# Performance work log

Hardware: AMD Instinct MI355X
Metric: run time of the kernel (lower is better)

## Reference

```python
import jax, jax.numpy as jnp
import numpy as np

N_NODES = 10000
N_EDGES = 640000
IN_FEATS = 128
H_FEATS1 = 128
NUM_OUTPUTS = 64


def setup_inputs() -> dict:
    key = jax.random.key(0)
    k0, k1, k2, k3, k4 = jax.random.split(key, 5)
    in_feat = jax.random.normal(k0, (N_NODES, IN_FEATS), dtype=jnp.float32)
    src = jax.random.randint(k1, (N_EDGES,), 0, N_NODES, dtype=jnp.int64)
    dst = jax.random.randint(k2, (N_EDGES,), 0, N_NODES, dtype=jnp.int64)
    W1 = jax.random.normal(k3, (IN_FEATS, H_FEATS1), dtype=jnp.float32) * 0.05
    b1 = jnp.zeros((H_FEATS1,), dtype=jnp.float32)
    W2 = jax.random.normal(k4, (H_FEATS1, NUM_OUTPUTS), dtype=jnp.float32) * 0.05
    b2 = jnp.zeros((NUM_OUTPUTS,), dtype=jnp.float32)
    return {"in_feat": in_feat, "src": src, "dst": dst,
            "W1": W1, "b1": b1, "W2": W2, "b2": b2}


def _graph_conv(src, dst, x, W, b):
    # DGL GraphConv with norm='both': out = D_out^{-1/2} A^T-agg D_in^{-1/2} x W + b
    n = x.shape[0]
    ones = jnp.ones((src.shape[0],), dtype=x.dtype)
    deg_out = jnp.clip(jax.ops.segment_sum(ones, src, num_segments=n), 1.0)
    deg_in = jnp.clip(jax.ops.segment_sum(ones, dst, num_segments=n), 1.0)
    h = x * jax.lax.rsqrt(deg_out)[:, None]            # src-side normalization
    agg = jax.ops.segment_sum(h[src], dst, num_segments=n)  # SpMM: sum over in-edges
    agg = agg * jax.lax.rsqrt(deg_in)[:, None]         # dst-side normalization
    return agg @ W + b


def reference(in_feat, src, dst, W1, b1, W2, b2):
    h = _graph_conv(src, dst, in_feat, W1, b1)
    h = jax.nn.relu(h)  # dropout=0 -> identity
    return _graph_conv(src, dst, h, W2, b2)
```

## Files before the change

kernel.cpp:

```cpp
#include <hip/hip_runtime.h>

#define NFEAT 128
#define NOUT  64
#define PCAP  128
#define HB    256

__global__ void hist_kernel(const int* __restrict__ src, const int* __restrict__ dst,
                            unsigned short* __restrict__ hist_src,
                            unsigned short* __restrict__ hist_dst,
                            unsigned int* __restrict__ pe, int nN, int nE) {
    extern __shared__ int bins[];
    int b = blockIdx.x;
    int per = (nE + HB - 1) / HB;
    int lo = b * per, hi = min(lo + per, nE);
    for (int i = threadIdx.x; i < nN; i += blockDim.x) bins[i] = 0;
    __syncthreads();
    for (int e = lo + threadIdx.x; e < hi; e += blockDim.x) {
        int s = src[e], d = dst[e];
        atomicAdd(&bins[d], 1);
        atomicAdd(&bins[s], 0x10000);
        pe[e] = (unsigned int)(unsigned short)s | ((unsigned int)d << 16);
    }
    __syncthreads();
    for (int i = threadIdx.x; i < nN; i += blockDim.x) {
        int v = bins[i];
        hist_dst[(size_t)b * nN + i] = (unsigned short)(v & 0xFFFF);
        hist_src[(size_t)b * nN + i] = (unsigned short)(v >> 16);
    }
}

__global__ void offsets_kernel(const unsigned short* __restrict__ hist_src,
                               const unsigned short* __restrict__ hist_dst,
                               unsigned short* __restrict__ base_rel,
                               unsigned short* __restrict__ deg_in,
                               float* __restrict__ rs_in, float* __restrict__ rs_out, int nN) {
    int tid = blockIdx.x * blockDim.x + threadIdx.x;
    if (tid < nN) {
        int i = tid;
        int run = 0;
#pragma unroll 16
        for (int b = 0; b < HB; b++) {
            base_rel[(size_t)b * nN + i] = (unsigned short)run;
            run += hist_dst[(size_t)b * nN + i];
        }
        deg_in[i] = (unsigned short)min(run, PCAP);
        rs_in[i] = rsqrtf(fmaxf((float)run, 1.0f));
    } else if (tid < 2 * nN) {
        int i = tid - nN;
        int to = 0;
#pragma unroll 16
        for (int b = 0; b < HB; b++) to += hist_src[(size_t)b * nN + i];
        rs_out[i] = rsqrtf(fmaxf((float)to, 1.0f));
    }
}

__global__ void scatter_kernel(const unsigned int* __restrict__ pe,
                               const unsigned short* __restrict__ base_rel,
                               unsigned short* __restrict__ csr, int nN, int nE) {
    extern __shared__ int cur[];
    int b = blockIdx.x;
    int per = (nE + HB - 1) / HB;
    int lo = b * per, hi = min(lo + per, nE);
    for (int i = threadIdx.x; i < nN; i += blockDim.x)
        cur[i] = base_rel[(size_t)b * nN + i];
    __syncthreads();
    for (int e = lo + threadIdx.x; e < hi; e += blockDim.x) {
        unsigned int v = pe[e];
        int s = v & 0xFFFF, d = v >> 16;
        int pos = atomicAdd(&cur[d], 1);
        if (pos < PCAP)
            csr[(size_t)d * PCAP + pos] = (unsigned short)s;
    }
}

__global__ void gather1_kernel(const unsigned short* __restrict__ deg_in,
                               const unsigned short* __restrict__ csr,
                               const float* __restrict__ x, const float* __restrict__ rs_out,
                               const float* __restrict__ rs_in,
                               float* __restrict__ t, int nN) {
    __shared__ unsigned short eids[4][PCAP];
    __shared__ float rsv[4][PCAP];
    int tid = threadIdx.x;
    int w = tid >> 6, lane = tid & 63;
    int i = blockIdx.x * 4 + w;
    int n = deg_in[i];
    ((unsigned int*)eids[w])[lane] = ((const unsigned int*)(csr + (size_t)i * PCAP))[lane];
    for (int e = lane; e < n; e += 64) rsv[w][e] = rs_out[eids[w][e]];

    const float4* xv = (const float4*)x;
    int quad = lane >> 4;
    int g = lane & 15;
    float s_in = rs_in[i];
#pragma unroll
    for (int p = 0; p < 2; p++) {
        int gg = g + 16 * p;
        float4 acc = {0.f, 0.f, 0.f, 0.f};
        int e = quad;
        for (; e + 28 < n; e += 32) {
            float4 vv[8]; float ff[8];
#pragma unroll
            for (int u = 0; u < 8; u++) {
                int s = eids[w][e + 4 * u];
                ff[u] = rsv[w][e + 4 * u];
                vv[u] = xv[(size_t)s * 32 + gg];
            }
#pragma unroll
            for (int u = 0; u < 8; u++) {
                acc.x += vv[u].x * ff[u];
                acc.y += vv[u].y * ff[u];
                acc.z += vv[u].z * ff[u];
                acc.w += vv[u].w * ff[u];
            }
        }
        for (; e + 12 < n; e += 16) {
            float4 vv[4]; float ff[4];
#pragma unroll
            for (int u = 0; u < 4; u++) {
                int s = eids[w][e + 4 * u];
                ff[u] = rsv[w][e + 4 * u];
                vv[u] = xv[(size_t)s * 32 + gg];
            }
#pragma unroll
            for (int u = 0; u < 4; u++) {
                acc.x += vv[u].x * ff[u];
                acc.y += vv[u].y * ff[u];
                acc.z += vv[u].z * ff[u];
                acc.w += vv[u].w * ff[u];
            }
        }
        for (; e < n; e += 4) {
            int s0 = eids[w][e];
            float f0 = rsv[w][e];
            float4 v0 = xv[(size_t)s0 * 32 + gg];
            acc.x += v0.x * f0; acc.y += v0.y * f0; acc.z += v0.z * f0; acc.w += v0.w * f0;
        }
#pragma unroll
        for (int d = 16; d <= 32; d <<= 1) {
            acc.x += __shfl_xor(acc.x, d);
            acc.y += __shfl_xor(acc.y, d);
            acc.z += __shfl_xor(acc.z, d);
            acc.w += __shfl_xor(acc.w, d);
        }
        if (lane < 16) {
            acc.x *= s_in; acc.y *= s_in; acc.z *= s_in; acc.w *= s_in;
            ((float4*)(t + (size_t)i * NFEAT))[gg] = acc;
        }
    }
}

#define NPB 16
__global__ void mlp_kernel(const float* __restrict__ t_in, const float* __restrict__ rs_out,
                           const float* __restrict__ W1, const float* __restrict__ b1,
                           const float* __restrict__ W2, float* __restrict__ z, int nN) {
    __shared__ float ts[NPB][NFEAT];
    __shared__ float h1[NPB][NFEAT];
    int i0 = blockIdx.x * NPB;
    int tid = threadIdx.x;
    for (int t2 = tid; t2 < NPB * NFEAT; t2 += 256)
        ts[t2 >> 7][t2 & 127] = t_in[(size_t)i0 * NFEAT + t2];
    __syncthreads();
    {
        int j = tid & 127;
        int g = (tid >> 7) * 8;
        float a[8];
        float b = b1[j];
#pragma unroll
        for (int u = 0; u < 8; u++) a[u] = b;
#pragma unroll 8
        for (int k = 0; k < NFEAT; k++) {
            float w = W1[k * NFEAT + j];
#pragma unroll
            for (int u = 0; u < 8; u++) a[u] += ts[g + u][k] * w;
        }
#pragma unroll
        for (int u = 0; u < 8; u++) h1[g + u][j] = fmaxf(a[u], 0.0f);
    }
    __syncthreads();
    {
        int j2 = tid & 63;
        int g2 = (tid >> 6) * 4;
        float c[4] = {0.f, 0.f, 0.f, 0.f};
#pragma unroll 8
        for (int k = 0; k < NFEAT; k++) {
            float w = W2[k * NOUT + j2];
#pragma unroll
            for (int u = 0; u < 4; u++) c[u] += h1[g2 + u][k] * w;
        }
#pragma unroll
        for (int u = 0; u < 4; u++)
            z[(size_t)(i0 + g2 + u) * NOUT + j2] = c[u] * rs_out[i0 + g2 + u];
    }
}

__global__ void gather2_kernel(const unsigned short* __restrict__ deg_in,
                               const unsigned short* __restrict__ csr,
                               const float* __restrict__ z, const float* __restrict__ rs_in,
                               const float* __restrict__ b2, float* __restrict__ out, int nN) {
    __shared__ unsigned short eids[4][PCAP];
    int tid = threadIdx.x;
    int w = tid >> 6, lane = tid & 63;
    int i = blockIdx.x * 4 + w;
    int n = deg_in[i];
    ((unsigned int*)eids[w])[lane] = ((const unsigned int*)(csr + (size_t)i * PCAP))[lane];

    const float4* zv = (const float4*)z;
    int quad = lane >> 4;
    int g = lane & 15;
    float4 acc = {0.f, 0.f, 0.f, 0.f};
    int e = quad;
    for (; e + 28 < n; e += 32) {
        float4 vv[8];
#pragma unroll
        for (int u = 0; u < 8; u++) {
            int s = eids[w][e + 4 * u];
            vv[u] = zv[(size_t)s * 16 + g];
        }
#pragma unroll
        for (int u = 0; u < 8; u++) {
            acc.x += vv[u].x; acc.y += vv[u].y; acc.z += vv[u].z; acc.w += vv[u].w;
        }
    }
    for (; e + 12 < n; e += 16) {
        float4 vv[4];
#pragma unroll
        for (int u = 0; u < 4; u++) {
            int s = eids[w][e + 4 * u];
            vv[u] = zv[(size_t)s * 16 + g];
        }
#pragma unroll
        for (int u = 0; u < 4; u++) {
            acc.x += vv[u].x; acc.y += vv[u].y; acc.z += vv[u].z; acc.w += vv[u].w;
        }
    }
    for (; e < n; e += 4) {
        float4 v0 = zv[(size_t)eids[w][e] * 16 + g];
        acc.x += v0.x; acc.y += v0.y; acc.z += v0.z; acc.w += v0.w;
    }
#pragma unroll
    for (int d = 16; d <= 32; d <<= 1) {
        acc.x += __shfl_xor(acc.x, d);
        acc.y += __shfl_xor(acc.y, d);
        acc.z += __shfl_xor(acc.z, d);
        acc.w += __shfl_xor(acc.w, d);
    }
    if (lane < 16) {
        float s = rs_in[i];
        float4 bb = ((const float4*)b2)[g];
        acc.x = acc.x * s + bb.x; acc.y = acc.y * s + bb.y;
        acc.z = acc.z * s + bb.z; acc.w = acc.w * s + bb.w;
        ((float4*)(out + (size_t)i * NOUT))[g] = acc;
    }
}

extern "C" void kernel_launch(void* const* d_in, const int* in_sizes, int n_in,
                              void* d_out, int out_size, void* d_ws, size_t ws_size,
                              hipStream_t stream) {
    const float* x  = (const float*)d_in[0];
    const int* src  = (const int*)d_in[1];
    const int* dst  = (const int*)d_in[2];
    const float* W1 = (const float*)d_in[3];
    const float* b1 = (const float*)d_in[4];
    const float* W2 = (const float*)d_in[5];
    const float* b2 = (const float*)d_in[6];
    float* out = (float*)d_out;

    const int nN = in_sizes[0] / NFEAT;
    const int nE = in_sizes[1];

    char* p = (char*)d_ws;
    unsigned short* hist_src = (unsigned short*)p; p += (size_t)HB * nN * 2;
    unsigned short* hist_dst = (unsigned short*)p; p += (size_t)HB * nN * 2;
    unsigned short* base_rel = (unsigned short*)p; p += (size_t)HB * nN * 2;
    unsigned int*   pe       = (unsigned int*)p;   p += (size_t)nE * 4;
    unsigned short* csr      = (unsigned short*)p; p += (size_t)nN * PCAP * 2;
    unsigned short* deg_in   = (unsigned short*)p; p += (size_t)nN * 2;
    float* rs_in  = (float*)p; p += (size_t)nN * sizeof(float);
    float* rs_out = (float*)p; p += (size_t)nN * sizeof(float);
    float* t = (float*)p; p += (size_t)nN * NFEAT * sizeof(float);
    float* z = (float*)p; p += (size_t)nN * NOUT * sizeof(float);

    hist_kernel<<<HB, 256, (size_t)nN * sizeof(int), stream>>>(
        src, dst, hist_src, hist_dst, pe, nN, nE);
    offsets_kernel<<<(2 * nN + 255) / 256, 256, 0, stream>>>(
        hist_src, hist_dst, base_rel, deg_in, rs_in, rs_out, nN);
    scatter_kernel<<<HB, 256, (size_t)nN * sizeof(int), stream>>>(
        pe, base_rel, csr, nN, nE);
    gather1_kernel<<<nN / 4, 256, 0, stream>>>(deg_in, csr, x, rs_out, rs_in, t, nN);
    mlp_kernel<<<nN / NPB, 256, 0, stream>>>(t, rs_out, W1, b1, W2, z, nN);
    gather2_kernel<<<nN / 4, 256, 0, stream>>>(deg_in, csr, z, rs_in, b2, out, nN);
}
```

Measured before the change: 160.3 us.

## Build CSR with global atomics in one pass, replacing histogram/offsets/scatter pipeline

Replaces the three-kernel, block-local histogram, prefix and scatter CSR construction with a memset plus a single kernel. That kernel does global atomic increments on the in and out degree arrays and writes each source index into a fixed-capacity per-destination slot. The rsqrt degree normalizations are now computed on the fly in the gather and MLP kernels instead of being precomputed. This removes two launches and large per-block histogram traffic, at the cost of contended global atomics. Neighbor order within each row also becomes nondeterministic, which changes the float summation order.

```diff
diff --git a/kernel.cpp b/kernel.cpp
--- a/kernel.cpp
+++ b/kernel.cpp
@@ -3,94 +3,39 @@
 #define NFEAT 128
 #define NOUT  64
 #define PCAP  128
-#define HB    256
-
-__global__ void hist_kernel(const int* __restrict__ src, const int* __restrict__ dst,
-                            unsigned short* __restrict__ hist_src,
-                            unsigned short* __restrict__ hist_dst,
-                            unsigned int* __restrict__ pe, int nN, int nE) {
-    extern __shared__ int bins[];
-    int b = blockIdx.x;
-    int per = (nE + HB - 1) / HB;
-    int lo = b * per, hi = min(lo + per, nE);
-    for (int i = threadIdx.x; i < nN; i += blockDim.x) bins[i] = 0;
-    __syncthreads();
-    for (int e = lo + threadIdx.x; e < hi; e += blockDim.x) {
+
+__global__ void build_kernel(const int* __restrict__ src, const int* __restrict__ dst,
+                             int* __restrict__ deg_in, int* __restrict__ deg_out,
+                             unsigned short* __restrict__ csr, int nE) {
+    int e = blockIdx.x * blockDim.x + threadIdx.x;
+    if (e < nE) {
         int s = src[e], d = dst[e];
-        atomicAdd(&bins[d], 1);
-        atomicAdd(&bins[s], 0x10000);
-        pe[e] = (unsigned int)(unsigned short)s | ((unsigned int)d << 16);
-    }
-    __syncthreads();
-    for (int i = threadIdx.x; i < nN; i += blockDim.x) {
-        int v = bins[i];
-        hist_dst[(size_t)b * nN + i] = (unsigned short)(v & 0xFFFF);
-        hist_src[(size_t)b * nN + i] = (unsigned short)(v >> 16);
-    }
-}
-
-__global__ void offsets_kernel(const unsigned short* __restrict__ hist_src,
-                               const unsigned short* __restrict__ hist_dst,
-                               unsigned short* __restrict__ base_rel,
-                               unsigned short* __restrict__ deg_in,
-                               float* __restrict__ rs_in, float* __restrict__ rs_out, int nN) {
-    int tid = blockIdx.x * blockDim.x + threadIdx.x;
-    if (tid < nN) {
-        int i = tid;
-        int run = 0;
-#pragma unroll 16
-        for (int b = 0; b < HB; b++) {
-            base_rel[(size_t)b * nN + i] = (unsigned short)run;
-            run += hist_dst[(size_t)b * nN + i];
-        }
-        deg_in[i] = (unsigned short)min(run, PCAP);
-        rs_in[i] = rsqrtf(fmaxf((float)run, 1.0f));
-    } else if (tid < 2 * nN) {
-        int i = tid - nN;
-        int to = 0;
-#pragma unroll 16
-        for (int b = 0; b < HB; b++) to += hist_src[(size_t)b * nN + i];
-        rs_out[i] = rsqrtf(fmaxf((float)to, 1.0f));
-    }
-}
-
-__global__ void scatter_kernel(const unsigned int* __restrict__ pe,
-                               const unsigned short* __restrict__ base_rel,
-                               unsigned short* __restrict__ csr, int nN, int nE) {
-    extern __shared__ int cur[];
-    int b = blockIdx.x;
-    int per = (nE + HB - 1) / HB;
-    int lo = b * per, hi = min(lo + per, nE);
-    for (int i = threadIdx.x; i < nN; i += blockDim.x)
-        cur[i] = base_rel[(size_t)b * nN + i];
-    __syncthreads();
-    for (int e = lo + threadIdx.x; e < hi; e += blockDim.x) {
-        unsigned int v = pe[e];
-        int s = v & 0xFFFF, d = v >> 16;
-        int pos = atomicAdd(&cur[d], 1);
+        atomicAdd(&deg_out[s], 1);
+        int pos = atomicAdd(&deg_in[d], 1);
         if (pos < PCAP)
             csr[(size_t)d * PCAP + pos] = (unsigned short)s;
     }
 }
 
-__global__ void gather1_kernel(const unsigned short* __restrict__ deg_in,
+__global__ void gather1_kernel(const int* __restrict__ deg_in, const int* __restrict__ deg_out,
                                const unsigned short* __restrict__ csr,
-                               const float* __restrict__ x, const float* __restrict__ rs_out,
-                               const float* __restrict__ rs_in,
+                               const float* __restrict__ x,
                                float* __restrict__ t, int nN) {
     __shared__ unsigned short eids[4][PCAP];
     __shared__ float rsv[4][PCAP];
     int tid = threadIdx.x;
     int w = tid >> 6, lane = tid & 63;
     int i = blockIdx.x * 4 + w;
-    int n = deg_in[i];
+    int nf = deg_in[i];
+    int n = min(nf, PCAP);
+    float s_in = rsqrtf(fmaxf((float)nf, 1.0f));
     ((unsigned int*)eids[w])[lane] = ((const unsigned int*)(csr + (size_t)i * PCAP))[lane];
-    for (int e = lane; e < n; e += 64) rsv[w][e] = rs_out[eids[w][e]];
+    for (int e = lane; e < n; e += 64)
+        rsv[w][e] = rsqrtf(fmaxf((float)deg_out[eids[w][e]], 1.0f));
 
     const float4* xv = (const float4*)x;
     int quad = lane >> 4;
     int g = lane & 15;
-    float s_in = rs_in[i];
 #pragma unroll
     for (int p = 0; p < 2; p++) {
         int gg = g + 16 * p;
@@ -149,7 +94,7 @@
 }
 
 #define NPB 16
-__global__ void mlp_kernel(const float* __restrict__ t_in, const float* __restrict__ rs_out,
+__global__ void mlp_kernel(const float* __restrict__ t_in, const int* __restrict__ deg_out,
                            const float* __restrict__ W1, const float* __restrict__ b1,
                            const float* __restrict__ W2, float* __restrict__ z, int nN) {
     __shared__ float ts[NPB][NFEAT];
@@ -187,20 +132,23 @@
             for (int u = 0; u < 4; u++) c[u] += h1[g2 + u][k] * w;
         }
 #pragma unroll
-        for (int u = 0; u < 4; u++)
-            z[(size_t)(i0 + g2 + u) * NOUT + j2] = c[u] * rs_out[i0 + g2 + u];
-    }
-}
-
-__global__ void gather2_kernel(const unsigned short* __restrict__ deg_in,
+        for (int u = 0; u < 4; u++) {
+            float rs = rsqrtf(fmaxf((float)deg_out[i0 + g2 + u], 1.0f));
+            z[(size_t)(i0 + g2 + u) * NOUT + j2] = c[u] * rs;
+        }
+    }
+}
+
+__global__ void gather2_kernel(const int* __restrict__ deg_in,
                                const unsigned short* __restrict__ csr,
-                               const float* __restrict__ z, const float* __restrict__ rs_in,
+                               const float* __restrict__ z,
                                const float* __restrict__ b2, float* __restrict__ out, int nN) {
     __shared__ unsigned short eids[4][PCAP];
     int tid = threadIdx.x;
     int w = tid >> 6, lane = tid & 63;
     int i = blockIdx.x * 4 + w;
-    int n = deg_in[i];
+    int nf = deg_in[i];
+    int n = min(nf, PCAP);
     ((unsigned int*)eids[w])[lane] = ((const unsigned int*)(csr + (size_t)i * PCAP))[lane];
 
     const float4* zv = (const float4*)z;
@@ -244,7 +192,7 @@
         acc.w += __shfl_xor(acc.w, d);
     }
     if (lane < 16) {
-        float s = rs_in[i];
+        float s = rsqrtf(fmaxf((float)nf, 1.0f));
         float4 bb = ((const float4*)b2)[g];
         acc.x = acc.x * s + bb.x; acc.y = acc.y * s + bb.y;
         acc.z = acc.z * s + bb.z; acc.w = acc.w * s + bb.w;
@@ -268,24 +216,15 @@
     const int nE = in_sizes[1];
 
     char* p = (char*)d_ws;
-    unsigned short* hist_src = (unsigned short*)p; p += (size_t)HB * nN * 2;
-    unsigned short* hist_dst = (unsigned short*)p; p += (size_t)HB * nN * 2;
-    unsigned short* base_rel = (unsigned short*)p; p += (size_t)HB * nN * 2;
-    unsigned int*   pe       = (unsigned int*)p;   p += (size_t)nE * 4;
-    unsigned short* csr      = (unsigned short*)p; p += (size_t)nN * PCAP * 2;
-    unsigned short* deg_in   = (unsigned short*)p; p += (size_t)nN * 2;
-    float* rs_in  = (float*)p; p += (size_t)nN * sizeof(float);
-    float* rs_out = (float*)p; p += (size_t)nN * sizeof(float);
+    int* deg_in  = (int*)p; p += (size_t)nN * sizeof(int);
+    int* deg_out = (int*)p; p += (size_t)nN * sizeof(int);
+    unsigned short* csr = (unsigned short*)p; p += (size_t)nN * PCAP * 2;
     float* t = (float*)p; p += (size_t)nN * NFEAT * sizeof(float);
     float* z = (float*)p; p += (size_t)nN * NOUT * sizeof(float);
 
-    hist_kernel<<<HB, 256, (size_t)nN * sizeof(int), stream>>>(
-        src, dst, hist_src, hist_dst, pe, nN, nE);
-    offsets_kernel<<<(2 * nN + 255) / 256, 256, 0, stream>>>(
-        hist_src, hist_dst, base_rel, deg_in, rs_in, rs_out, nN);
-    scatter_kernel<<<HB, 256, (size_t)nN * sizeof(int), stream>>>(
-        pe, base_rel, csr, nN, nE);
-    gather1_kernel<<<nN / 4, 256, 0, stream>>>(deg_in, csr, x, rs_out, rs_in, t, nN);
-    mlp_kernel<<<nN / NPB, 256, 0, stream>>>(t, rs_out, W1, b1, W2, z, nN);
-    gather2_kernel<<<nN / 4, 256, 0, stream>>>(deg_in, csr, z, rs_in, b2, out, nN);
-}
+    hipMemsetAsync(d_ws, 0, 2 * (size_t)nN * sizeof(int), stream);
+    build_kernel<<<(nE + 255) / 256, 256, 0, stream>>>(src, dst, deg_in, deg_out, csr, nE);
+    gather1_kernel<<<nN / 4, 256, 0, stream>>>(deg_in, deg_out, csr, x, t, nN);
+    mlp_kernel<<<nN / NPB, 256, 0, stream>>>(t, deg_out, W1, b1, W2, z, nN);
+    gather2_kernel<<<nN / 4, 256, 0, stream>>>(deg_in, csr, z, b2, out, nN);
+}
```

Measured after the change: 179.4 us. +11.9%, slower.

## Store gathered node features in fp16 to halve gather traffic

Applied to the files above, without the earlier changes.

Converts the input features to fp16 inside the histogram kernel and has the MLP write its per-node output in fp16. Both gather kernels then read half as many bytes per edge, with each lane handling eight values instead of four and accumulating in fp32. This targets memory bandwidth in the two SpMM gathers, which are random-access and bandwidth-bound. The trade is reduced precision in the aggregated features and an extra conversion pass over x in the first kernel.

```diff
diff --git a/kernel.cpp b/kernel.cpp
--- a/kernel.cpp
+++ b/kernel.cpp
@@ -1,4 +1,5 @@
 #include <hip/hip_runtime.h>
+#include <hip/hip_fp16.h>
 
 #define NFEAT 128
 #define NOUT  64
@@ -8,7 +9,9 @@
 __global__ void hist_kernel(const int* __restrict__ src, const int* __restrict__ dst,
                             unsigned short* __restrict__ hist_src,
                             unsigned short* __restrict__ hist_dst,
-                            unsigned int* __restrict__ pe, int nN, int nE) {
+                            unsigned int* __restrict__ pe,
+                            const float* __restrict__ x, uint4* __restrict__ xh,
+                            int nN, int nE) {
     extern __shared__ int bins[];
     int b = blockIdx.x;
     int per = (nE + HB - 1) / HB;
@@ -26,6 +29,14 @@
         int v = bins[i];
         hist_dst[(size_t)b * nN + i] = (unsigned short)(v & 0xFFFF);
         hist_src[(size_t)b * nN + i] = (unsigned short)(v >> 16);
+    }
+    const float4* xf = (const float4*)x;
+    int nchunk = nN * NFEAT / 8;
+    for (int c = blockIdx.x * blockDim.x + threadIdx.x; c < nchunk; c += gridDim.x * blockDim.x) {
+        float4 a = xf[2 * c], bb = xf[2 * c + 1];
+        __half2 h[4] = {__floats2half2_rn(a.x, a.y),  __floats2half2_rn(a.z, a.w),
+                        __floats2half2_rn(bb.x, bb.y), __floats2half2_rn(bb.z, bb.w)};
+        xh[c] = *(uint4*)h;
     }
 }
 
@@ -73,9 +84,17 @@
     }
 }
 
+__device__ __forceinline__ void fma8(float* acc, uint4 v, float f) {
+    const __half2* h = (const __half2*)&v;
+    float2 p0 = __half22float2(h[0]), p1 = __half22float2(h[1]);
+    float2 p2 = __half22float2(h[2]), p3 = __half22float2(h[3]);
+    acc[0] += p0.x * f; acc[1] += p0.y * f; acc[2] += p1.x * f; acc[3] += p1.y * f;
+    acc[4] += p2.x * f; acc[5] += p2.y * f; acc[6] += p3.x * f; acc[7] += p3.y * f;
+}
+
 __global__ void gather1_kernel(const unsigned short* __restrict__ deg_in,
                                const unsigned short* __restrict__ csr,
-                               const float* __restrict__ x, const float* __restrict__ rs_out,
+                               const uint4* __restrict__ xh, const float* __restrict__ rs_out,
                                const float* __restrict__ rs_in,
                                float* __restrict__ t, int nN) {
     __shared__ unsigned short eids[4][PCAP];
@@ -87,71 +106,52 @@
     ((unsigned int*)eids[w])[lane] = ((const unsigned int*)(csr + (size_t)i * PCAP))[lane];
     for (int e = lane; e < n; e += 64) rsv[w][e] = rs_out[eids[w][e]];
 
-    const float4* xv = (const float4*)x;
     int quad = lane >> 4;
     int g = lane & 15;
     float s_in = rs_in[i];
-#pragma unroll
-    for (int p = 0; p < 2; p++) {
-        int gg = g + 16 * p;
-        float4 acc = {0.f, 0.f, 0.f, 0.f};
-        int e = quad;
-        for (; e + 28 < n; e += 32) {
-            float4 vv[8]; float ff[8];
-#pragma unroll
-            for (int u = 0; u < 8; u++) {
-                int s = eids[w][e + 4 * u];
-                ff[u] = rsv[w][e + 4 * u];
-                vv[u] = xv[(size_t)s * 32 + gg];
-            }
-#pragma unroll
-            for (int u = 0; u < 8; u++) {
-                acc.x += vv[u].x * ff[u];
-                acc.y += vv[u].y * ff[u];
-                acc.z += vv[u].z * ff[u];
-                acc.w += vv[u].w * ff[u];
-            }
-        }
-        for (; e + 12 < n; e += 16) {
-            float4 vv[4]; float ff[4];
-#pragma unroll
-            for (int u = 0; u < 4; u++) {
-                int s = eids[w][e + 4 * u];
-                ff[u] = rsv[w][e + 4 * u];
-                vv[u] = xv[(size_t)s * 32 + gg];
-            }
-#pragma unroll
-            for (int u = 0; u < 4; u++) {
-                acc.x += vv[u].x * ff[u];
-                acc.y += vv[u].y * ff[u];
-                acc.z += vv[u].z * ff[u];
-                acc.w += vv[u].w * ff[u];
-            }
-        }
-        for (; e < n; e += 4) {
-            int s0 = eids[w][e];
-            float f0 = rsv[w][e];
-            float4 v0 = xv[(size_t)s0 * 32 + gg];
-            acc.x += v0.x * f0; acc.y += v0.y * f0; acc.z += v0.z * f0; acc.w += v0.w * f0;
-        }
-#pragma unroll
-        for (int d = 16; d <= 32; d <<= 1) {
-            acc.x += __shfl_xor(acc.x, d);
-            acc.y += __shfl_xor(acc.y, d);
-            acc.z += __shfl_xor(acc.z, d);
-            acc.w += __shfl_xor(acc.w, d);
-        }
-        if (lane < 16) {
-            acc.x *= s_in; acc.y *= s_in; acc.z *= s_in; acc.w *= s_in;
-            ((float4*)(t + (size_t)i * NFEAT))[gg] = acc;
-        }
+    float acc[8] = {0.f, 0.f, 0.f, 0.f, 0.f, 0.f, 0.f, 0.f};
+    int e = quad;
+    for (; e + 28 < n; e += 32) {
+        uint4 vv[8]; float ff[8];
+#pragma unroll
+        for (int u = 0; u < 8; u++) {
+            int s = eids[w][e + 4 * u];
+            ff[u] = rsv[w][e + 4 * u];
+            vv[u] = xh[(size_t)s * 16 + g];
+        }
+#pragma unroll
+        for (int u = 0; u < 8; u++) fma8(acc, vv[u], ff[u]);
+    }
+    for (; e + 12 < n; e += 16) {
+        uint4 vv[4]; float ff[4];
+#pragma unroll
+        for (int u = 0; u < 4; u++) {
+            int s = eids[w][e + 4 * u];
+            ff[u] = rsv[w][e + 4 * u];
+            vv[u] = xh[(size_t)s * 16 + g];
+        }
+#pragma unroll
+        for (int u = 0; u < 4; u++) fma8(acc, vv[u], ff[u]);
+    }
+    for (; e < n; e += 4) {
+        fma8(acc, xh[(size_t)eids[w][e] * 16 + g], rsv[w][e]);
+    }
+#pragma unroll
+    for (int d = 16; d <= 32; d <<= 1)
+#pragma unroll
+        for (int k = 0; k < 8; k++) acc[k] += __shfl_xor(acc[k], d);
+    if (lane < 16) {
+        float4 o0 = {acc[0] * s_in, acc[1] * s_in, acc[2] * s_in, acc[3] * s_in};
+        float4 o1 = {acc[4] * s_in, acc[5] * s_in, acc[6] * s_in, acc[7] * s_in};
+        float4* tp = (float4*)(t + (size_t)i * NFEAT + g * 8);
+        tp[0] = o0; tp[1] = o1;
     }
 }
 
 #define NPB 16
 __global__ void mlp_kernel(const float* __restrict__ t_in, const float* __restrict__ rs_out,
                            const float* __restrict__ W1, const float* __restrict__ b1,
-                           const float* __restrict__ W2, float* __restrict__ z, int nN) {
+                           const float* __restrict__ W2, __half* __restrict__ zh, int nN) {
     __shared__ float ts[NPB][NFEAT];
     __shared__ float h1[NPB][NFEAT];
     int i0 = blockIdx.x * NPB;
@@ -188,13 +188,13 @@
         }
 #pragma unroll
         for (int u = 0; u < 4; u++)
-            z[(size_t)(i0 + g2 + u) * NOUT + j2] = c[u] * rs_out[i0 + g2 + u];
+            zh[(size_t)(i0 + g2 + u) * NOUT + j2] = __float2half_rn(c[u] * rs_out[i0 + g2 + u]);
     }
 }
 
 __global__ void gather2_kernel(const unsigned short* __restrict__ deg_in,
                                const unsigned short* __restrict__ csr,
-                               const float* __restrict__ z, const float* __restrict__ rs_in,
+                               const uint4* __restrict__ zh, const float* __restrict__ rs_in,
                                const float* __restrict__ b2, float* __restrict__ out, int nN) {
     __shared__ unsigned short eids[4][PCAP];
     int tid = threadIdx.x;
@@ -203,52 +203,38 @@
     int n = deg_in[i];
     ((unsigned int*)eids[w])[lane] = ((const unsigned int*)(csr + (size_t)i * PCAP))[lane];
 
-    const float4* zv = (const float4*)z;
-    int quad = lane >> 4;
-    int g = lane & 15;
-    float4 acc = {0.f, 0.f, 0.f, 0.f};
-    int e = quad;
-    for (; e + 28 < n; e += 32) {
-        float4 vv[8];
-#pragma unroll
-        for (int u = 0; u < 8; u++) {
-            int s = eids[w][e + 4 * u];
-            vv[u] = zv[(size_t)s * 16 + g];
-        }
-#pragma unroll
-        for (int u = 0; u < 8; u++) {
-            acc.x += vv[u].x; acc.y += vv[u].y; acc.z += vv[u].z; acc.w += vv[u].w;
-        }
-    }
-    for (; e + 12 < n; e += 16) {
-        float4 vv[4];
-#pragma unroll
-        for (int u = 0; u < 4; u++) {
-            int s = eids[w][e + 4 * u];
-            vv[u] = zv[(size_t)s * 16 + g];
-        }
-#pragma unroll
-        for (int u = 0; u < 4; u++) {
-            acc.x += vv[u].x; acc.y += vv[u].y; acc.z += vv[u].z; acc.w += vv[u].w;
-        }
-    }
-    for (; e < n; e += 4) {
-        float4 v0 = zv[(size_t)eids[w][e] * 16 + g];
-        acc.x += v0.x; acc.y += v0.y; acc.z += v0.z; acc.w += v0.w;
-    }
-#pragma unroll
-    for (int d = 16; d <= 32; d <<= 1) {
-        acc.x += __shfl_xor(acc.x, d);
-        acc.y += __shfl_xor(acc.y, d);
-        acc.z += __shfl_xor(acc.z, d);
-        acc.w += __shfl_xor(acc.w, d);
-    }
-    if (lane < 16) {
+    int oct = lane >> 3;
+    int g = lane & 7;
+    float acc[8] = {0.f, 0.f, 0.f, 0.f, 0.f, 0.f, 0.f, 0.f};
+    int e = oct;
+    for (; e + 56 < n; e += 64) {
+        uint4 vv[8];
+#pragma unroll
+        for (int u = 0; u < 8; u++) vv[u] = zh[(size_t)eids[w][e + 8 * u] * 8 + g];
+#pragma unroll
+        for (int u = 0; u < 8; u++) fma8(acc, vv[u], 1.0f);
+    }
+    for (; e + 24 < n; e += 32) {
+        uint4 vv[4];
+#pragma unroll
+        for (int u = 0; u < 4; u++) vv[u] = zh[(size_t)eids[w][e + 8 * u] * 8 + g];
+#pragma unroll
+        for (int u = 0; u < 4; u++) fma8(acc, vv[u], 1.0f);
+    }
+    for (; e < n; e += 8) {
+        fma8(acc, zh[(size_t)eids[w][e] * 8 + g], 1.0f);
+    }
+#pragma unroll
+    for (int d = 8; d <= 32; d <<= 1)
+#pragma unroll
+        for (int k = 0; k < 8; k++) acc[k] += __shfl_xor(acc[k], d);
+    if (lane < 8) {
         float s = rs_in[i];
-        float4 bb = ((const float4*)b2)[g];
-        acc.x = acc.x * s + bb.x; acc.y = acc.y * s + bb.y;
-        acc.z = acc.z * s + bb.z; acc.w = acc.w * s + bb.w;
-        ((float4*)(out + (size_t)i * NOUT))[g] = acc;
+        float4 bb0 = ((const float4*)b2)[2 * g], bb1 = ((const float4*)b2)[2 * g + 1];
+        float4 o0 = {acc[0] * s + bb0.x, acc[1] * s + bb0.y, acc[2] * s + bb0.z, acc[3] * s + bb0.w};
+        float4 o1 = {acc[4] * s + bb1.x, acc[5] * s + bb1.y, acc[6] * s + bb1.z, acc[7] * s + bb1.w};
+        float4* op = (float4*)(out + (size_t)i * NOUT + g * 8);
+        op[0] = o0; op[1] = o1;
     }
 }
 
@@ -276,16 +262,17 @@
     unsigned short* deg_in   = (unsigned short*)p; p += (size_t)nN * 2;
     float* rs_in  = (float*)p; p += (size_t)nN * sizeof(float);
     float* rs_out = (float*)p; p += (size_t)nN * sizeof(float);
+    uint4* xh = (uint4*)p; p += (size_t)nN * NFEAT * 2;
     float* t = (float*)p; p += (size_t)nN * NFEAT * sizeof(float);
-    float* z = (float*)p; p += (size_t)nN * NOUT * sizeof(float);
+    __half* zh = (__half*)p; p += (size_t)nN * NOUT * 2;
 
     hist_kernel<<<HB, 256, (size_t)nN * sizeof(int), stream>>>(
-        src, dst, hist_src, hist_dst, pe, nN, nE);
+        src, dst, hist_src, hist_dst, pe, x, xh, nN, nE);
     offsets_kernel<<<(2 * nN + 255) / 256, 256, 0, stream>>>(
         hist_src, hist_dst, base_rel, deg_in, rs_in, rs_out, nN);
     scatter_kernel<<<HB, 256, (size_t)nN * sizeof(int), stream>>>(
         pe, base_rel, csr, nN, nE);
-    gather1_kernel<<<nN / 4, 256, 0, stream>>>(deg_in, csr, x, rs_out, rs_in, t, nN);
-    mlp_kernel<<<nN / NPB, 256, 0, stream>>>(t, rs_out, W1, b1, W2, z, nN);
-    gather2_kernel<<<nN / 4, 256, 0, stream>>>(deg_in, csr, z, rs_in, b2, out, nN);
-}
+    gather1_kernel<<<nN / 4, 256, 0, stream>>>(deg_in, csr, xh, rs_out, rs_in, t, nN);
+    mlp_kernel<<<nN / NPB, 256, 0, stream>>>(t, rs_out, W1, b1, W2, zh, nN);
+    gather2_kernel<<<nN / 4, 256, 0, stream>>>(deg_in, csr, (const uint4*)zh, rs_in, b2, out, nN);
+}
```

Result: faster. 153.9 us (-4.0%).
